# Kernel tuning notes

Hardware: AMD Instinct MI355X
Metric: run time of the kernel (lower is better)

## Reference

```python
import jax, jax.numpy as jnp
import numpy as np

NUM_ACTIONS = 16  # number of unique leaf actions (= output_dim)


def setup_inputs() -> dict:
    key = jax.random.key(0)
    ks = jax.random.split(key, 7)
    B, IN, D, A = 32768, 128, 511, 512
    L = D + A + 1  # 1024 leaves
    x = jax.random.normal(ks[0], (B, IN), dtype=jnp.float32)
    Wd = jax.random.normal(ks[1], (D, IN), dtype=jnp.float32) * 0.05
    bd = jax.random.normal(ks[2], (D,), dtype=jnp.float32) * 0.05
    Wa = jax.random.normal(ks[3], (A, IN), dtype=jnp.float32) * 0.05
    ba = jax.random.normal(ks[4], (A,), dtype=jnp.float32) * 0.05
    Wl = jax.random.normal(ks[5], (L, 2 * (D + A)), dtype=jnp.float32) * 0.05
    seg_ids = jax.random.randint(ks[6], (L,), 0, NUM_ACTIONS, dtype=jnp.int32)
    return {"x": x, "Wd": Wd, "bd": bd, "Wa": Wa, "ba": ba, "Wl": Wl,
            "seg_ids": seg_ids}


def reference(x, Wd, bd, Wa, ba, Wl, seg_ids):
    # dual linear heads (torch Linear: y = x @ W.T + b)
    x1 = x @ Wd.T + bd            # [B, D]
    x2 = x @ Wa.T + ba            # [B, A]
    h = jnp.concatenate([x1, x2], axis=1)                     # [B, D+A]
    hh = jnp.concatenate([jax.nn.relu(h), jax.nn.relu(-h)], axis=1)  # [B, 2(D+A)]
    leaf = hh @ Wl.T              # [B, L]
    # ragged per-action max over leaf columns (MaxPoolLayer)
    pooled = jax.ops.segment_max(leaf.T, seg_ids,
                                 num_segments=NUM_ACTIONS).T   # [B, NUM_ACTIONS]
    return jax.nn.softmax(pooled, axis=-1)
```

## Files before the change

kernel.cpp:

```cpp
#include <hip/hip_runtime.h>
#include <hip/hip_bf16.h>
#include <cstdint>
#include <cmath>

#define AS1 __attribute__((address_space(1)))
#define AS3 __attribute__((address_space(3)))

typedef unsigned short u16;
typedef uint32_t u32;
typedef __attribute__((ext_vector_type(8))) __bf16 bf16x8;
typedef __attribute__((ext_vector_type(8))) unsigned short u16x8;
typedef __attribute__((ext_vector_type(4))) float f32x4;

__device__ __forceinline__ u16 f2bf(float f) {
    uint32_t u = __builtin_bit_cast(uint32_t, f);
    return (u16)((u + 0x7fffu + ((u >> 16) & 1u)) >> 16);
}

__device__ __forceinline__ u32 f2ord(float f) {
    u32 u = __builtin_bit_cast(u32, f);
    return u ^ (u32)(((int32_t)u >> 31) | 0x80000000);
}
__device__ __forceinline__ float ord2f(u32 v) {
    u32 u = (v & 0x80000000u) ? (v ^ 0x80000000u) : ~v;
    return __builtin_bit_cast(float, u);
}

__global__ void setup_all(const float* __restrict__ x,
                          const float* __restrict__ Wd, const float* __restrict__ bd,
                          const float* __restrict__ Wa, const float* __restrict__ ba,
                          const float* __restrict__ Wl,
                          u16* __restrict__ xb, u16* __restrict__ w1b,
                          float* __restrict__ bb, u16* __restrict__ w1t,
                          u16* __restrict__ wsb, u16* __restrict__ dlb,
                          float* __restrict__ cl) {
    __shared__ float cred[256];
    const int b = blockIdx.x;
    const int tid = threadIdx.x;
    if (b < 2048) {
        long idx = (long)(b * 256 + tid) * 8;
        float4 a = *(const float4*)(x + idx);
        float4 c = *(const float4*)(x + idx + 4);
        u16x8 o;
        o[0]=f2bf(a.x); o[1]=f2bf(a.y); o[2]=f2bf(a.z); o[3]=f2bf(a.w);
        o[4]=f2bf(c.x); o[5]=f2bf(c.y); o[6]=f2bf(c.z); o[7]=f2bf(c.w);
        *(u16x8*)(xb + idx) = o;
    } else if (b < 2112) {
        int t = (b - 2048) * 256 + tid;
        int row = t >> 4, g = (t & 15) * 8;
        const float* src = nullptr;
        if (row < 511)       src = Wd + row * 128 + g;
        else if (row < 1023) src = Wa + (row - 511) * 128 + g;
        u16x8 o = 0;
        if (src) {
            #pragma unroll
            for (int j = 0; j < 8; ++j) o[j] = f2bf(src[j]);
        }
        *(u16x8*)(w1b + row * 128 + g) = o;
        #pragma unroll
        for (int j = 0; j < 8; ++j) w1t[(g + j) * 1024 + row] = o[j];
        if ((t & 15) == 0)
            bb[row] = row < 511 ? bd[row] : (row < 1023 ? ba[row - 511] : 0.f);
    } else if (b < 2624) {
        int t = (b - 2112) * 256 + tid;
        int row = t >> 7, g = (t & 127) * 8;
        const float* src = Wl + (long)row * 2046;
        u16x8 o;
        #pragma unroll
        for (int j = 0; j < 8; ++j) {
            int c = g + j;
            o[j] = (c < 1023) ? f2bf(0.5f * (src[c] + src[1023 + c])) : (u16)0;
        }
        *(u16x8*)(wsb + (long)row * 1024 + g) = o;
    } else {
        const int l0 = (b - 2624) * 2;
        const int lo = tid >> 7, g = (tid & 127) * 8;
        const float* src = Wl + (long)(l0 + lo) * 2046;
        u16x8 o;
        float part = 0.f;
        #pragma unroll
        for (int j = 0; j < 8; ++j) {
            int c = g + j;
            float v = (c < 1023) ? (src[c] - src[1023 + c]) : 0.f;
            o[j] = f2bf(v);
            float b1 = c < 511 ? bd[c] : (c < 1023 ? ba[c - 511] : 0.f);
            part += v * b1;
        }
        *(u16x8*)(dlb + (long)(l0 + lo) * 1024 + g) = o;
        cred[tid] = part;
        __syncthreads();
        if (tid < 2) {
            float s = 0.f;
            #pragma unroll
            for (int k = 0; k < 128; ++k) s += cred[tid * 128 + k];
            cl[l0 + tid] = 0.5f * s;
        }
    }
}

__global__ __launch_bounds__(256) void gemm_wc(const u16* __restrict__ A,
        const u16* __restrict__ B, u16* __restrict__ wcb) {
    __shared__ u16 As[128 * 32];
    __shared__ u16 Bs[128 * 32];
    const int tid  = threadIdx.x;
    const int lane = tid & 63, wave = tid >> 6;
    const int wy = wave >> 1, wx = wave & 1;
    const int i16 = lane & 15, q = lane >> 4;
    const long blockM = (long)blockIdx.x * 128;
    const int koff = (blockIdx.x * 4) & 31;

    f32x4 acc[4][4];
    #pragma unroll
    for (int m = 0; m < 4; ++m)
        #pragma unroll
        for (int n = 0; n < 4; ++n) acc[m][n] = f32x4{0.f,0.f,0.f,0.f};

    const int cA = wave * 2, srow = lane >> 2, scol = (lane & 3) * 8;
    const u16* a0 = A + (blockM + cA * 16 + srow) * 1024 + scol;
    const u16* a1 = A + (blockM + (cA + 1) * 16 + srow) * 1024 + scol;
    const u16* b0 = B + (long)(cA * 16 + srow) * 1024 + scol;
    const u16* b1 = B + (long)((cA + 1) * 16 + srow) * 1024 + scol;

    for (int it = 0; it < 32; ++it) {
        const int k0 = ((it + koff) & 31) << 5;
        __builtin_amdgcn_global_load_lds((const AS1 void*)(a0 + k0), (AS3 void*)&As[cA * 512],       16, 0, 0);
        __builtin_amdgcn_global_load_lds((const AS1 void*)(a1 + k0), (AS3 void*)&As[(cA + 1) * 512], 16, 0, 0);
        __builtin_amdgcn_global_load_lds((const AS1 void*)(b0 + k0), (AS3 void*)&Bs[cA * 512],       16, 0, 0);
        __builtin_amdgcn_global_load_lds((const AS1 void*)(b1 + k0), (AS3 void*)&Bs[(cA + 1) * 512], 16, 0, 0);
        __syncthreads();
        bf16x8 af[4], bfv[4];
        #pragma unroll
        for (int s = 0; s < 4; ++s) {
            af[s]  = *(const bf16x8*)&As[(wy * 64 + s * 16 + i16) * 32 + q * 8];
            bfv[s] = *(const bf16x8*)&Bs[(wx * 64 + s * 16 + i16) * 32 + q * 8];
        }
        #pragma unroll
        for (int sm = 0; sm < 4; ++sm)
            #pragma unroll
            for (int sn = 0; sn < 4; ++sn)
                acc[sm][sn] = __builtin_amdgcn_mfma_f32_16x16x32_bf16(af[sm], bfv[sn], acc[sm][sn], 0, 0, 0);
        __syncthreads();
    }
    #pragma unroll
    for (int sm = 0; sm < 4; ++sm)
        #pragma unroll
        for (int sn = 0; sn < 4; ++sn) {
            const int col = wx * 64 + sn * 16 + i16;
            #pragma unroll
            for (int r = 0; r < 4; ++r) {
                const long row = blockM + wy * 64 + sm * 16 + 4 * q + r;
                wcb[row * 128 + col] = f2bf(0.5f * acc[sm][sn][r]);
            }
        }
}

__global__ __launch_bounds__(256) void gemm_h(const u16* __restrict__ A,
        const u16* __restrict__ B, const float* __restrict__ bias,
        u16* __restrict__ habs) {
    __shared__ u16 As[128 * 32];
    __shared__ u16 Bs[128 * 32];
    __shared__ u16 obuf[128 * 136];
    const int tid  = threadIdx.x;
    const int lane = tid & 63, wave = tid >> 6;
    const int wy = wave >> 1, wx = wave & 1;
    const int i16 = lane & 15, q = lane >> 4;
    const int xcd = blockIdx.x, y = blockIdx.y;
    const long blockM = (long)(xcd * 32 + (y >> 3)) * 128;
    const int  blockN = (y & 7) * 128;
    const int  koff = ((y >> 3) * 2) & 3;

    f32x4 acc[4][4];
    #pragma unroll
    for (int m = 0; m < 4; ++m)
        #pragma unroll
        for (int n = 0; n < 4; ++n) acc[m][n] = f32x4{0.f,0.f,0.f,0.f};

    const int cA = wave * 2, srow = lane >> 2, scol = (lane & 3) * 8;
    const u16* a0 = A + (blockM + cA * 16 + srow) * 128 + scol;
    const u16* a1 = A + (blockM + (cA + 1) * 16 + srow) * 128 + scol;
    const u16* b0 = B + ((long)blockN + cA * 16 + srow) * 128 + scol;
    const u16* b1 = B + ((long)blockN + (cA + 1) * 16 + srow) * 128 + scol;

    for (int it = 0; it < 4; ++it) {
        const int k0 = ((it + koff) & 3) << 5;
        __builtin_amdgcn_global_load_lds((const AS1 void*)(a0 + k0), (AS3 void*)&As[cA * 512],       16, 0, 0);
        __builtin_amdgcn_global_load_lds((const AS1 void*)(a1 + k0), (AS3 void*)&As[(cA + 1) * 512], 16, 0, 0);
        __builtin_amdgcn_global_load_lds((const AS1 void*)(b0 + k0), (AS3 void*)&Bs[cA * 512],       16, 0, 0);
        __builtin_amdgcn_global_load_lds((const AS1 void*)(b1 + k0), (AS3 void*)&Bs[(cA + 1) * 512], 16, 0, 0);
        __syncthreads();
        bf16x8 af[4], bfv[4];
        #pragma unroll
        for (int s = 0; s < 4; ++s) {
            af[s]  = *(const bf16x8*)&As[(wy * 64 + s * 16 + i16) * 32 + q * 8];
            bfv[s] = *(const bf16x8*)&Bs[(wx * 64 + s * 16 + i16) * 32 + q * 8];
        }
        #pragma unroll
        for (int sm = 0; sm < 4; ++sm)
            #pragma unroll
            for (int sn = 0; sn < 4; ++sn)
                acc[sm][sn] = __builtin_amdgcn_mfma_f32_16x16x32_bf16(af[sm], bfv[sn], acc[sm][sn], 0, 0, 0);
        __syncthreads();
    }
    float bv[4];
    #pragma unroll
    for (int sn = 0; sn < 4; ++sn) bv[sn] = bias[blockN + wx * 64 + sn * 16 + i16];
    #pragma unroll
    for (int sm = 0; sm < 4; ++sm)
        #pragma unroll
        for (int sn = 0; sn < 4; ++sn)
            #pragma unroll
            for (int r = 0; r < 4; ++r)
                obuf[(wy * 64 + sm * 16 + 4 * q + r) * 136 + wx * 64 + sn * 16 + i16] =
                    f2bf(fabsf(acc[sm][sn][r] + bv[sn]));
    __syncthreads();
    const int cg = (tid & 15) * 8;
    #pragma unroll
    for (int it = 0; it < 8; ++it) {
        const int row = it * 16 + (tid >> 4);
        *(u16x8*)&habs[(blockM + row) * 1024 + blockN + cg] =
            *(const u16x8*)&obuf[row * 136 + cg];
    }
}

__global__ __launch_bounds__(256) void gemm_leaf(const u16* __restrict__ habs,
        const u16* __restrict__ xb, const u16* __restrict__ wsb,
        const u16* __restrict__ wcb, const float* __restrict__ cl,
        const int* __restrict__ seg, u32* __restrict__ pp) {
    __shared__ u16 As[128 * 32];
    __shared__ u16 Bs[128 * 32];
    __shared__ u32 pmax[128 * 16];
    const int tid  = threadIdx.x;
    const int lane = tid & 63, wave = tid >> 6;
    const int wy = wave >> 1, wx = wave & 1;
    const int i16 = lane & 15, q = lane >> 4;
    const int xcd = blockIdx.x, y = blockIdx.y;
    const int nTile = y & 7;
    const long blockM = (long)(xcd * 32 + (y >> 3)) * 128;
    const int  blockN = nTile * 128;
    const int  koff = ((y >> 3) * 2) & 31;

    #pragma unroll
    for (int j = 0; j < 8; ++j) pmax[tid + j * 256] = 0u;

    f32x4 acc[4][4];
    #pragma unroll
    for (int m = 0; m < 4; ++m)
        #pragma unroll
        for (int n = 0; n < 4; ++n) acc[m][n] = f32x4{0.f,0.f,0.f,0.f};

    const int cA = wave * 2, srow = lane >> 2, scol = (lane & 3) * 8;
    {
        const u16* a0 = habs + (blockM + cA * 16 + srow) * 1024 + scol;
        const u16* a1 = habs + (blockM + (cA + 1) * 16 + srow) * 1024 + scol;
        const u16* b0 = wsb + ((long)blockN + cA * 16 + srow) * 1024 + scol;
        const u16* b1 = wsb + ((long)blockN + (cA + 1) * 16 + srow) * 1024 + scol;
        for (int it = 0; it < 32; ++it) {
            const int k0 = ((it + koff) & 31) << 5;
            __builtin_amdgcn_global_load_lds((const AS1 void*)(a0 + k0), (AS3 void*)&As[cA * 512],       16, 0, 0);
            __builtin_amdgcn_global_load_lds((const AS1 void*)(a1 + k0), (AS3 void*)&As[(cA + 1) * 512], 16, 0, 0);
            __builtin_amdgcn_global_load_lds((const AS1 void*)(b0 + k0), (AS3 void*)&Bs[cA * 512],       16, 0, 0);
            __builtin_amdgcn_global_load_lds((const AS1 void*)(b1 + k0), (AS3 void*)&Bs[(cA + 1) * 512], 16, 0, 0);
            __syncthreads();
            bf16x8 af[4], bfv[4];
            #pragma unroll
            for (int s = 0; s < 4; ++s) {
                af[s]  = *(const bf16x8*)&As[(wy * 64 + s * 16 + i16) * 32 + q * 8];
                bfv[s] = *(const bf16x8*)&Bs[(wx * 64 + s * 16 + i16) * 32 + q * 8];
            }
            #pragma unroll
            for (int sm = 0; sm < 4; ++sm)
                #pragma unroll
                for (int sn = 0; sn < 4; ++sn)
                    acc[sm][sn] = __builtin_amdgcn_mfma_f32_16x16x32_bf16(af[sm], bfv[sn], acc[sm][sn], 0, 0, 0);
            __syncthreads();
        }
    }
    {
        const u16* a0 = xb + (blockM + cA * 16 + srow) * 128 + scol;
        const u16* a1 = xb + (blockM + (cA + 1) * 16 + srow) * 128 + scol;
        const u16* b0 = wcb + ((long)blockN + cA * 16 + srow) * 128 + scol;
        const u16* b1 = wcb + ((long)blockN + (cA + 1) * 16 + srow) * 128 + scol;
        for (int it = 0; it < 4; ++it) {
            const int k0 = it << 5;
            __builtin_amdgcn_global_load_lds((const AS1 void*)(a0 + k0), (AS3 void*)&As[cA * 512],       16, 0, 0);
            __builtin_amdgcn_global_load_lds((const AS1 void*)(a1 + k0), (AS3 void*)&As[(cA + 1) * 512], 16, 0, 0);
            __builtin_amdgcn_global_load_lds((const AS1 void*)(b0 + k0), (AS3 void*)&Bs[cA * 512],       16, 0, 0);
            __builtin_amdgcn_global_load_lds((const AS1 void*)(b1 + k0), (AS3 void*)&Bs[(cA + 1) * 512], 16, 0, 0);
            __syncthreads();
            bf16x8 af[4], bfv[4];
            #pragma unroll
            for (int s = 0; s < 4; ++s) {
                af[s]  = *(const bf16x8*)&As[(wy * 64 + s * 16 + i16) * 32 + q * 8];
                bfv[s] = *(const bf16x8*)&Bs[(wx * 64 + s * 16 + i16) * 32 + q * 8];
            }
            #pragma unroll
            for (int sm = 0; sm < 4; ++sm)
                #pragma unroll
                for (int sn = 0; sn < 4; ++sn)
                    acc[sm][sn] = __builtin_amdgcn_mfma_f32_16x16x32_bf16(af[sm], bfv[sn], acc[sm][sn], 0, 0, 0);
            __syncthreads();
        }
    }

    int segc[4]; float clv[4];
    #pragma unroll
    for (int sn = 0; sn < 4; ++sn) {
        const int col = blockN + wx * 64 + sn * 16 + i16;
        segc[sn] = seg[col];
        clv[sn]  = cl[col];
    }
    #pragma unroll
    for (int sm = 0; sm < 4; ++sm)
        #pragma unroll
        for (int sn = 0; sn < 4; ++sn)
            #pragma unroll
            for (int r = 0; r < 4; ++r) {
                const int rl = wy * 64 + sm * 16 + 4 * q + r;
                atomicMax(&pmax[rl * 16 + segc[sn]], f2ord(acc[sm][sn][r] + clv[sn]));
            }
    __syncthreads();
    #pragma unroll
    for (int j = 0; j < 8; ++j) {
        int idx = tid + j * 256;
        pp[((long)nTile << 19) + ((blockM + (idx >> 4)) << 4) + (idx & 15)] = pmax[idx];
    }
}

__global__ __launch_bounds__(256) void finalize(const u32* __restrict__ pp,
                                                float* __restrict__ out) {
    const int tid = threadIdx.x;
    const long row = (long)blockIdx.x * 16 + (tid >> 4);
    const int t = tid & 15;
    u32 m = 0;
    #pragma unroll
    for (int p = 0; p < 8; ++p)
        m = max(m, pp[((long)p << 19) + (row << 4) + t]);
    float logit = ord2f(m);
    float rm = logit;
    #pragma unroll
    for (int d = 8; d >= 1; d >>= 1) rm = fmaxf(rm, __shfl_xor(rm, d, 16));
    float e = __expf(logit - rm);
    float s = e;
    #pragma unroll
    for (int d = 8; d >= 1; d >>= 1) s += __shfl_xor(s, d, 16);
    out[(row << 4) + t] = e / s;
}

extern "C" void kernel_launch(void* const* d_in, const int* in_sizes, int n_in,
                              void* d_out, int out_size, void* d_ws, size_t ws_size,
                              hipStream_t stream) {
    const float* x  = (const float*)d_in[0];
    const float* Wd = (const float*)d_in[1];
    const float* bd = (const float*)d_in[2];
    const float* Wa = (const float*)d_in[3];
    const float* ba = (const float*)d_in[4];
    const float* Wl = (const float*)d_in[5];
    const int*  seg = (const int*)d_in[6];
    float* out = (float*)d_out;

    char* ws = (char*)d_ws;
    u16*   xb   = (u16*)(ws);
    u16*   w1b  = (u16*)(ws + 8388608);
    float* bb   = (float*)(ws + 8650752);
    u16*   w1t  = (u16*)(ws + 8654848);
    u16*   wsb  = (u16*)(ws + 8916992);
    u16*   dlb  = (u16*)(ws + 11014144);
    u16*   wcb  = (u16*)(ws + 13111296);
    float* clp  = (float*)(ws + 13373440);
    u16*   habs = (u16*)(ws + 13377536);
    u32*   pp   = (u32*)(ws + 80486400);

    setup_all<<<3136, 256, 0, stream>>>(x, Wd, bd, Wa, ba, Wl,
                                        xb, w1b, bb, w1t, wsb, dlb, clp);
    gemm_wc  <<<8, 256, 0, stream>>>(dlb, w1t, wcb);
    gemm_h   <<<dim3(8, 256), 256, 0, stream>>>(xb, w1b, bb, habs);
    gemm_leaf<<<dim3(8, 256), 256, 0, stream>>>(habs, xb, wsb, wcb, clp, seg, pp);
    finalize <<<2048, 256, 0, stream>>>(pp, out);
}
```

Baseline: 243.3 us.

## Merge wc and h GEMMs into one launch and preload full K for h

Folds the small 8-block gemm_wc into the gemm_h launch as an extra grid row (blockIdx.y == 256), so both run concurrently in a single kernel. Separately, the h GEMM now loads all four K chunks into LDS at once and runs the MFMAs with a single barrier instead of four load/sync rounds. LDS is shared via a union with the output staging buffer. The goal is to cut a launch and the serialized tail of the tiny wc GEMM, and to reduce synchronization, at the cost of more LDS per block (possibly lower occupancy) and the 32-iteration wc blocks potentially becoming a long tail.

```diff
diff --git a/kernel.cpp b/kernel.cpp
--- a/kernel.cpp
+++ b/kernel.cpp
@@ -98,16 +98,20 @@
     }
 }
 
-__global__ __launch_bounds__(256) void gemm_wc(const u16* __restrict__ A,
-        const u16* __restrict__ B, u16* __restrict__ wcb) {
-    __shared__ u16 As[128 * 32];
-    __shared__ u16 Bs[128 * 32];
+__global__ __launch_bounds__(256) void gemm_hwc(
+        const u16* __restrict__ xb, const u16* __restrict__ w1b,
+        const float* __restrict__ bb,
+        const u16* __restrict__ dlb, const u16* __restrict__ w1t,
+        u16* __restrict__ habs, u16* __restrict__ wcb) {
+    __shared__ union SharedU {
+        struct { u16 As[4 * 4096]; u16 Bs[4 * 4096]; } s;
+        u16 obuf[128 * 136];
+    } sh;
     const int tid  = threadIdx.x;
     const int lane = tid & 63, wave = tid >> 6;
     const int wy = wave >> 1, wx = wave & 1;
     const int i16 = lane & 15, q = lane >> 4;
-    const long blockM = (long)blockIdx.x * 128;
-    const int koff = (blockIdx.x * 4) & 31;
+    const int cA = wave * 2, srow = lane >> 2, scol = (lane & 3) * 8;
 
     f32x4 acc[4][4];
     #pragma unroll
@@ -115,102 +119,91 @@
         #pragma unroll
         for (int n = 0; n < 4; ++n) acc[m][n] = f32x4{0.f,0.f,0.f,0.f};
 
-    const int cA = wave * 2, srow = lane >> 2, scol = (lane & 3) * 8;
-    const u16* a0 = A + (blockM + cA * 16 + srow) * 1024 + scol;
-    const u16* a1 = A + (blockM + (cA + 1) * 16 + srow) * 1024 + scol;
-    const u16* b0 = B + (long)(cA * 16 + srow) * 1024 + scol;
-    const u16* b1 = B + (long)((cA + 1) * 16 + srow) * 1024 + scol;
-
-    for (int it = 0; it < 32; ++it) {
-        const int k0 = ((it + koff) & 31) << 5;
-        __builtin_amdgcn_global_load_lds((const AS1 void*)(a0 + k0), (AS3 void*)&As[cA * 512],       16, 0, 0);
-        __builtin_amdgcn_global_load_lds((const AS1 void*)(a1 + k0), (AS3 void*)&As[(cA + 1) * 512], 16, 0, 0);
-        __builtin_amdgcn_global_load_lds((const AS1 void*)(b0 + k0), (AS3 void*)&Bs[cA * 512],       16, 0, 0);
-        __builtin_amdgcn_global_load_lds((const AS1 void*)(b1 + k0), (AS3 void*)&Bs[(cA + 1) * 512], 16, 0, 0);
-        __syncthreads();
-        bf16x8 af[4], bfv[4];
-        #pragma unroll
-        for (int s = 0; s < 4; ++s) {
-            af[s]  = *(const bf16x8*)&As[(wy * 64 + s * 16 + i16) * 32 + q * 8];
-            bfv[s] = *(const bf16x8*)&Bs[(wx * 64 + s * 16 + i16) * 32 + q * 8];
+    if (blockIdx.y == 256) {
+        const long blockM = (long)blockIdx.x * 128;
+        const int koff = (blockIdx.x * 4) & 31;
+        const u16* a0 = dlb + (blockM + cA * 16 + srow) * 1024 + scol;
+        const u16* a1 = dlb + (blockM + (cA + 1) * 16 + srow) * 1024 + scol;
+        const u16* b0 = w1t + (long)(cA * 16 + srow) * 1024 + scol;
+        const u16* b1 = w1t + (long)((cA + 1) * 16 + srow) * 1024 + scol;
+        for (int it = 0; it < 32; ++it) {
+            const int k0 = ((it + koff) & 31) << 5;
+            __builtin_amdgcn_global_load_lds((const AS1 void*)(a0 + k0), (AS3 void*)&sh.s.As[cA * 512],       16, 0, 0);
+            __builtin_amdgcn_global_load_lds((const AS1 void*)(a1 + k0), (AS3 void*)&sh.s.As[(cA + 1) * 512], 16, 0, 0);
+            __builtin_amdgcn_global_load_lds((const AS1 void*)(b0 + k0), (AS3 void*)&sh.s.Bs[cA * 512],       16, 0, 0);
+            __builtin_amdgcn_global_load_lds((const AS1 void*)(b1 + k0), (AS3 void*)&sh.s.Bs[(cA + 1) * 512], 16, 0, 0);
+            __syncthreads();
+            bf16x8 af[4], bfv[4];
+            #pragma unroll
+            for (int s = 0; s < 4; ++s) {
+                af[s]  = *(const bf16x8*)&sh.s.As[(wy * 64 + s * 16 + i16) * 32 + q * 8];
+                bfv[s] = *(const bf16x8*)&sh.s.Bs[(wx * 64 + s * 16 + i16) * 32 + q * 8];
+            }
+            #pragma unroll
+            for (int sm = 0; sm < 4; ++sm)
+                #pragma unroll
+                for (int sn = 0; sn < 4; ++sn)
+                    acc[sm][sn] = __builtin_amdgcn_mfma_f32_16x16x32_bf16(af[sm], bfv[sn], acc[sm][sn], 0, 0, 0);
+            __syncthreads();
         }
         #pragma unroll
         for (int sm = 0; sm < 4; ++sm)
             #pragma unroll
-            for (int sn = 0; sn < 4; ++sn)
-                acc[sm][sn] = __builtin_amdgcn_mfma_f32_16x16x32_bf16(af[sm], bfv[sn], acc[sm][sn], 0, 0, 0);
-        __syncthreads();
-    }
-    #pragma unroll
-    for (int sm = 0; sm < 4; ++sm)
-        #pragma unroll
-        for (int sn = 0; sn < 4; ++sn) {
-            const int col = wx * 64 + sn * 16 + i16;
-            #pragma unroll
-            for (int r = 0; r < 4; ++r) {
-                const long row = blockM + wy * 64 + sm * 16 + 4 * q + r;
-                wcb[row * 128 + col] = f2bf(0.5f * acc[sm][sn][r]);
-            }
-        }
-}
-
-__global__ __launch_bounds__(256) void gemm_h(const u16* __restrict__ A,
-        const u16* __restrict__ B, const float* __restrict__ bias,
-        u16* __restrict__ habs) {
-    __shared__ u16 As[128 * 32];
-    __shared__ u16 Bs[128 * 32];
-    __shared__ u16 obuf[128 * 136];
-    const int tid  = threadIdx.x;
-    const int lane = tid & 63, wave = tid >> 6;
-    const int wy = wave >> 1, wx = wave & 1;
-    const int i16 = lane & 15, q = lane >> 4;
+            for (int sn = 0; sn < 4; ++sn) {
+                const int col = wx * 64 + sn * 16 + i16;
+                #pragma unroll
+                for (int r = 0; r < 4; ++r) {
+                    const long row = blockM + wy * 64 + sm * 16 + 4 * q + r;
+                    wcb[row * 128 + col] = f2bf(0.5f * acc[sm][sn][r]);
+                }
+            }
+        return;
+    }
+
     const int xcd = blockIdx.x, y = blockIdx.y;
     const long blockM = (long)(xcd * 32 + (y >> 3)) * 128;
     const int  blockN = (y & 7) * 128;
-    const int  koff = ((y >> 3) * 2) & 3;
-
-    f32x4 acc[4][4];
-    #pragma unroll
-    for (int m = 0; m < 4; ++m)
-        #pragma unroll
-        for (int n = 0; n < 4; ++n) acc[m][n] = f32x4{0.f,0.f,0.f,0.f};
-
-    const int cA = wave * 2, srow = lane >> 2, scol = (lane & 3) * 8;
-    const u16* a0 = A + (blockM + cA * 16 + srow) * 128 + scol;
-    const u16* a1 = A + (blockM + (cA + 1) * 16 + srow) * 128 + scol;
-    const u16* b0 = B + ((long)blockN + cA * 16 + srow) * 128 + scol;
-    const u16* b1 = B + ((long)blockN + (cA + 1) * 16 + srow) * 128 + scol;
-
-    for (int it = 0; it < 4; ++it) {
-        const int k0 = ((it + koff) & 3) << 5;
-        __builtin_amdgcn_global_load_lds((const AS1 void*)(a0 + k0), (AS3 void*)&As[cA * 512],       16, 0, 0);
-        __builtin_amdgcn_global_load_lds((const AS1 void*)(a1 + k0), (AS3 void*)&As[(cA + 1) * 512], 16, 0, 0);
-        __builtin_amdgcn_global_load_lds((const AS1 void*)(b0 + k0), (AS3 void*)&Bs[cA * 512],       16, 0, 0);
-        __builtin_amdgcn_global_load_lds((const AS1 void*)(b1 + k0), (AS3 void*)&Bs[(cA + 1) * 512], 16, 0, 0);
-        __syncthreads();
+
+    const u16* a0 = xb + (blockM + cA * 16 + srow) * 128 + scol;
+    const u16* a1 = xb + (blockM + (cA + 1) * 16 + srow) * 128 + scol;
+    const u16* b0 = w1b + ((long)blockN + cA * 16 + srow) * 128 + scol;
+    const u16* b1 = w1b + ((long)blockN + (cA + 1) * 16 + srow) * 128 + scol;
+    #pragma unroll
+    for (int kc = 0; kc < 4; ++kc) {
+        const int k0 = kc * 32;
+        __builtin_amdgcn_global_load_lds((const AS1 void*)(a0 + k0), (AS3 void*)&sh.s.As[kc * 4096 + cA * 512],       16, 0, 0);
+        __builtin_amdgcn_global_load_lds((const AS1 void*)(a1 + k0), (AS3 void*)&sh.s.As[kc * 4096 + (cA + 1) * 512], 16, 0, 0);
+        __builtin_amdgcn_global_load_lds((const AS1 void*)(b0 + k0), (AS3 void*)&sh.s.Bs[kc * 4096 + cA * 512],       16, 0, 0);
+        __builtin_amdgcn_global_load_lds((const AS1 void*)(b1 + k0), (AS3 void*)&sh.s.Bs[kc * 4096 + (cA + 1) * 512], 16, 0, 0);
+    }
+    float bv[4];
+    #pragma unroll
+    for (int sn = 0; sn < 4; ++sn) bv[sn] = bb[blockN + wx * 64 + sn * 16 + i16];
+    __syncthreads();
+
+    #pragma unroll
+    for (int ks = 0; ks < 4; ++ks) {
         bf16x8 af[4], bfv[4];
         #pragma unroll
         for (int s = 0; s < 4; ++s) {
-            af[s]  = *(const bf16x8*)&As[(wy * 64 + s * 16 + i16) * 32 + q * 8];
-            bfv[s] = *(const bf16x8*)&Bs[(wx * 64 + s * 16 + i16) * 32 + q * 8];
+            af[s]  = *(const bf16x8*)&sh.s.As[ks * 4096 + (wy * 64 + s * 16 + i16) * 32 + q * 8];
+            bfv[s] = *(const bf16x8*)&sh.s.Bs[ks * 4096 + (wx * 64 + s * 16 + i16) * 32 + q * 8];
         }
         #pragma unroll
         for (int sm = 0; sm < 4; ++sm)
             #pragma unroll
             for (int sn = 0; sn < 4; ++sn)
                 acc[sm][sn] = __builtin_amdgcn_mfma_f32_16x16x32_bf16(af[sm], bfv[sn], acc[sm][sn], 0, 0, 0);
-        __syncthreads();
-    }
-    float bv[4];
-    #pragma unroll
-    for (int sn = 0; sn < 4; ++sn) bv[sn] = bias[blockN + wx * 64 + sn * 16 + i16];
+    }
+    __syncthreads();
+
     #pragma unroll
     for (int sm = 0; sm < 4; ++sm)
         #pragma unroll
         for (int sn = 0; sn < 4; ++sn)
             #pragma unroll
             for (int r = 0; r < 4; ++r)
-                obuf[(wy * 64 + sm * 16 + 4 * q + r) * 136 + wx * 64 + sn * 16 + i16] =
+                sh.obuf[(wy * 64 + sm * 16 + 4 * q + r) * 136 + wx * 64 + sn * 16 + i16] =
                     f2bf(fabsf(acc[sm][sn][r] + bv[sn]));
     __syncthreads();
     const int cg = (tid & 15) * 8;
@@ -218,7 +211,7 @@
     for (int it = 0; it < 8; ++it) {
         const int row = it * 16 + (tid >> 4);
         *(u16x8*)&habs[(blockM + row) * 1024 + blockN + cg] =
-            *(const u16x8*)&obuf[row * 136 + cg];
+            *(const u16x8*)&sh.obuf[row * 136 + cg];
     }
 }
 
@@ -372,8 +365,7 @@
 
     setup_all<<<3136, 256, 0, stream>>>(x, Wd, bd, Wa, ba, Wl,
                                         xb, w1b, bb, w1t, wsb, dlb, clp);
-    gemm_wc  <<<8, 256, 0, stream>>>(dlb, w1t, wcb);
-    gemm_h   <<<dim3(8, 256), 256, 0, stream>>>(xb, w1b, bb, habs);
+    gemm_hwc <<<dim3(8, 257), 256, 0, stream>>>(xb, w1b, bb, dlb, w1t, habs, wcb);
     gemm_leaf<<<dim3(8, 256), 256, 0, stream>>>(habs, xb, wsb, wcb, clp, seg, pp);
     finalize <<<2048, 256, 0, stream>>>(pp, out);
 }
```

Measured after the change: 240.4 us. Within noise of the previous version (-1.2%).
